# Optimization experiments

Measured on AMD Instinct MI355X. Metric: run time of the kernel, lower is better.

The kernel has to match this reference:

```python
import jax, jax.numpy as jnp
import numpy as np

N, T, DM = 8192, 32, 128   # nodes, patches, d_model (d_in = T*DM = 4096)
M, NNZ = 1024, 131072      # hyperedges, incidences
EPS = 1e-5
SLOPE = 0.2


def _bn(x, g, b, axes):
    # BatchNorm with batch statistics (training-mode math, eval dropout)
    m = jnp.mean(x, axis=axes, keepdims=True)
    v = jnp.var(x, axis=axes, keepdims=True)
    return (x - m) / jnp.sqrt(v + EPS) * g + b


def _hconv(x, he_attr, he_n, he_e, W, att, bias, heads):
    # PyG HypergraphConv, use_attention=True, attention_mode='node', concat=False
    out = W.shape[1] // heads
    xt = (x @ W).reshape(N, heads, out)          # [N, H, F]
    et = (he_attr @ W).reshape(M, heads, out)    # [M, H, F]
    xi = xt[he_n]                                # [nnz, H, F] gather node feats
    ej = et[he_e]                                # [nnz, H, F] gather edge feats
    alpha = jnp.sum(jnp.concatenate([xi, ej], axis=-1) * att, axis=-1)  # [nnz, H]
    alpha = jax.nn.leaky_relu(alpha, SLOPE)
    # segment softmax grouped by hyperedge (attention_mode='node')
    amax = jax.ops.segment_max(alpha, he_e, num_segments=M)
    ex = jnp.exp(alpha - amax[he_e])
    alpha = ex / jax.ops.segment_sum(ex, he_e, num_segments=M)[he_e]
    # degree normalizers (hyperedge_weight == 1)
    ones = jnp.ones((NNZ,), x.dtype)
    Dn = jax.ops.segment_sum(ones, he_n, num_segments=N)
    Dinv = jnp.where(Dn > 0, 1.0 / Dn, 0.0)
    Bm = jax.ops.segment_sum(ones, he_e, num_segments=M)
    Binv = jnp.where(Bm > 0, 1.0 / Bm, 0.0)
    # node -> edge, then edge -> node message passing
    eo = jax.ops.segment_sum(alpha[:, :, None] * Binv[he_e][:, None, None] * xi,
                             he_e, num_segments=M)                     # [M, H, F]
    no = jax.ops.segment_sum(alpha[:, :, None] * Dinv[he_n][:, None, None] * eo[he_e],
                             he_n, num_segments=N)                     # [N, H, F]
    return no.mean(axis=1) + bias  # concat=False -> mean over heads


def setup_inputs() -> dict:
    key = jax.random.key(0)
    ks = jax.random.split(key, 16)
    d_in = T * DM
    s = 0.02
    inp = {
        "x": jax.random.normal(ks[0], (N, T, DM), jnp.float32),
        "he_nodes": jax.random.randint(ks[1], (NNZ,), 0, N),
        "he_edges": jax.random.randint(ks[2], (NNZ,), 0, M),
        "W1": jax.random.normal(ks[3], (d_in, DM), jnp.float32) * s,
        "b1": jnp.zeros((DM,), jnp.float32),
        "g1": jnp.ones((DM,), jnp.float32), "be1": jnp.zeros((DM,), jnp.float32),
        "Wh1": jax.random.normal(ks[4], (DM, 4 * DM), jnp.float32) * s,
        "att1": jax.random.normal(ks[5], (1, 4, 2 * DM), jnp.float32) * s,
        "bh1": jnp.zeros((DM,), jnp.float32),
        "g2": jnp.ones((DM,), jnp.float32), "be2": jnp.zeros((DM,), jnp.float32),
        "Wh2": jax.random.normal(ks[6], (DM, DM), jnp.float32) * s,
        "att2": jax.random.normal(ks[7], (1, 1, 2 * DM), jnp.float32) * s,
        "bh2": jnp.zeros((DM,), jnp.float32),
        "g3": jnp.ones((DM,), jnp.float32), "be3": jnp.zeros((DM,), jnp.float32),
        "W3": jax.random.normal(ks[8], (DM, d_in), jnp.float32) * s,
        "b3": jnp.zeros((d_in,), jnp.float32),
        "g4": jnp.ones((DM,), jnp.float32), "be4": jnp.zeros((DM,), jnp.float32),
    }
    return inp


def reference(x, he_nodes, he_edges, W1, b1, g1, be1, Wh1, att1, bh1,
              g2, be2, Wh2, att2, bh2, g3, be3, W3, b3, g4, be4):
    src = x
    h = x.reshape(N, T * DM)
    h = jax.nn.leaky_relu(h @ W1 + b1, SLOPE)
    h = _bn(h, g1, be1, 0)
    # hyperedge_attr = incidence^T @ h  (== to_dense_adj(...).T @ h)
    he_attr = jax.ops.segment_sum(h[he_nodes], he_edges, num_segments=M)
    h = h + _hconv(h, he_attr, he_nodes, he_edges, Wh1, att1, bh1, 4)
    h = _bn(h, g2, be2, 0)
    he_attr = jax.ops.segment_sum(h[he_nodes], he_edges, num_segments=M)
    h = h + _hconv(h, he_attr, he_nodes, he_edges, Wh2, att2, bh2, 1)
    h = _bn(h, g3, be3, 0)
    h = jax.nn.leaky_relu(h @ W3 + b3, SLOPE)
    h = src + h.reshape(N, T, DM)
    h = _bn(h, g4, be4, (0, 1))  # BN over channel DM, stats over (N, T)
    return h
```

## Files before the change

kernel.cpp:

```cpp
#include <hip/hip_runtime.h>
#include <hip/hip_bf16.h>
#include <math.h>

#define NN   8192
#define TT   32
#define DIN  4096
#define MME  1024
#define NNZK 131072
#define EPSV 1e-5f
#define MALL (NN + MME)

typedef __attribute__((ext_vector_type(8))) short bf16x8;
typedef __attribute__((ext_vector_type(4))) float f32x4;

__device__ __forceinline__ float lrelu(float v){ return v > 0.f ? v : 0.2f*v; }
__device__ __forceinline__ short f2b(float f){
    union { __hip_bfloat16 h; short s; } u; u.h = __float2bfloat16(f); return u.s;
}

__global__ void zero_i(int* p, int n){ int i = blockIdx.x*256 + threadIdx.x; if (i < n) p[i] = 0; }
__global__ void zero_f(float* p, int n){ int i = blockIdx.x*256 + threadIdx.x; if (i < n) p[i] = 0.f; }
__global__ void copy_i(const int* a, int* b, int n){ int i = blockIdx.x*256 + threadIdx.x; if (i < n) b[i] = a[i]; }

__global__ void count_seg(const int* __restrict__ he_n, const int* __restrict__ he_e,
                          int* __restrict__ ncnt, int* __restrict__ ecnt){
    int k = blockIdx.x*256 + threadIdx.x;
    if (k < NNZK){ atomicAdd(&ecnt[he_e[k]], 1); atomicAdd(&ncnt[he_n[k]], 1); }
}

__global__ void scan_excl(const int* __restrict__ cnt, int* __restrict__ off, int n){
    __shared__ int buf[1024];
    __shared__ int carry;
    int t = threadIdx.x;
    if (t == 0) carry = 0;
    __syncthreads();
    for (int base = 0; base < n; base += 1024){
        int i = base + t;
        int v = (i < n) ? cnt[i] : 0;
        buf[t] = v; __syncthreads();
        for (int s = 1; s < 1024; s <<= 1){
            int tmp = (t >= s) ? buf[t - s] : 0;
            __syncthreads();
            buf[t] += tmp;
            __syncthreads();
        }
        if (i < n) off[i] = carry + buf[t] - v;
        __syncthreads();
        if (t == 1023) carry += buf[1023];
        __syncthreads();
    }
    if (t == 0) off[n] = carry;
}

__global__ void fill_perm(const int* __restrict__ seg, int* __restrict__ cur, int* __restrict__ perm){
    int k = blockIdx.x*256 + threadIdx.x;
    if (k < NNZK){ int p = atomicAdd(&cur[seg[k]], 1); perm[p] = k; }
}

__global__ void wconv_t(const float* __restrict__ W, __hip_bfloat16* __restrict__ BT, int K, int N){
    __shared__ float tile[32][33];
    int k0 = blockIdx.y*32, n0 = blockIdx.x*32;
    int tx = threadIdx.x & 31, ty = threadIdx.x >> 5;
    for (int i = ty; i < 32; i += 8) tile[i][tx] = W[(size_t)(k0+i)*N + n0+tx];
    __syncthreads();
    for (int i = ty; i < 32; i += 8)
        BT[(size_t)(n0+i)*K + k0 + tx] = __float2bfloat16(tile[tx][i]);
}

#define SWZ(b) ((b) ^ ((((b) >> 6) & 7) << 4))

template<int MODE>
__global__ __launch_bounds__(256) void gemm_nt(
    const float* __restrict__ Aact, const __hip_bfloat16* __restrict__ Bwt,
    float* __restrict__ C, const float* __restrict__ bias, const float* __restrict__ add,
    const float* __restrict__ coef, int M, int N, int K, int kchunk)
{
    __shared__ f32x4 WsRaw[512];
    __shared__ f32x4 XsRaw[512];
    char* Ws = (char*)WsRaw;
    char* Xs = (char*)XsRaw;
    const int tid = threadIdx.x;
    const int lane = tid & 63;
    const int w = tid >> 6;
    const int m0 = blockIdx.y << 7, n0 = blockIdx.x << 7;
    const int kz = blockIdx.z * kchunk;
    const int wN = (w >> 1) << 6, wM = (w & 1) << 6;

    const int s0 = tid, s1 = tid + 256;
    const int r0 = s0 >> 2, k0b = (s0 & 3) << 3;
    const int r1 = s1 >> 2, k1b = (s1 & 3) << 3;
    const float* pX0 = Aact + (size_t)(m0 + r0)*K + kz + k0b;
    const float* pX1 = Aact + (size_t)(m0 + r1)*K + kz + k1b;
    const __hip_bfloat16* pW0 = Bwt + (size_t)(n0 + r0)*K + kz + k0b;
    const __hip_bfloat16* pW1 = Bwt + (size_t)(n0 + r1)*K + kz + k1b;
    const int wo0 = SWZ(s0 << 4), wo1 = SWZ(s1 << 4);

    int rwOff[4], rxOff[4];
#pragma unroll
    for (int f = 0; f < 4; f++){
        rwOff[f] = SWZ((wN + f*16 + (lane & 15))*64 + ((lane >> 4) << 4));
        rxOff[f] = SWZ((wM + f*16 + (lane & 15))*64 + ((lane >> 4) << 4));
    }

    f32x4 acc[4][4] = {};

    float4 x0l = *(const float4*)pX0, x0h = *(const float4*)(pX0+4);
    float4 x1l = *(const float4*)pX1, x1h = *(const float4*)(pX1+4);
    bf16x8 w0 = *(const bf16x8*)pW0, w1 = *(const bf16x8*)pW1;

    const int nsteps = kchunk >> 5;
    for (int ks = 0; ks < nsteps; ks++){
        bf16x8 vx0, vx1;
        vx0[0]=f2b(x0l.x); vx0[1]=f2b(x0l.y); vx0[2]=f2b(x0l.z); vx0[3]=f2b(x0l.w);
        vx0[4]=f2b(x0h.x); vx0[5]=f2b(x0h.y); vx0[6]=f2b(x0h.z); vx0[7]=f2b(x0h.w);
        vx1[0]=f2b(x1l.x); vx1[1]=f2b(x1l.y); vx1[2]=f2b(x1l.z); vx1[3]=f2b(x1l.w);
        vx1[4]=f2b(x1h.x); vx1[5]=f2b(x1h.y); vx1[6]=f2b(x1h.z); vx1[7]=f2b(x1h.w);
        __syncthreads();
        *(bf16x8*)(Xs + wo0) = vx0;
        *(bf16x8*)(Xs + wo1) = vx1;
        *(bf16x8*)(Ws + wo0) = w0;
        *(bf16x8*)(Ws + wo1) = w1;
        __syncthreads();
        if (ks + 1 < nsteps){
            pX0 += 32; pX1 += 32; pW0 += 32; pW1 += 32;
            x0l = *(const float4*)pX0; x0h = *(const float4*)(pX0+4);
            x1l = *(const float4*)pX1; x1h = *(const float4*)(pX1+4);
            w0 = *(const bf16x8*)pW0;  w1 = *(const bf16x8*)pW1;
        }
        bf16x8 wf[4], xf[4];
#pragma unroll
        for (int f = 0; f < 4; f++){
            wf[f] = *(const bf16x8*)(Ws + rwOff[f]);
            xf[f] = *(const bf16x8*)(Xs + rxOff[f]);
        }
#pragma unroll
        for (int i = 0; i < 4; i++)
#pragma unroll
            for (int j = 0; j < 4; j++)
                acc[i][j] = __builtin_amdgcn_mfma_f32_16x16x32_bf16(wf[i], xf[j], acc[i][j], 0, 0, 0);
    }

    const int mc = wM + (lane & 15);
    const int ncb = wN + ((lane >> 4) << 2);
    float* Cz = (MODE == 0) ? C + (size_t)blockIdx.z * ((size_t)M * (size_t)N) : C;
#pragma unroll
    for (int j = 0; j < 4; j++){
        int row = m0 + mc + j*16;
#pragma unroll
        for (int i = 0; i < 4; i++){
            int col = n0 + ncb + i*16;
            f32x4 v = acc[i][j];
            if (MODE == 1){
                float4 b4 = *(const float4*)&bias[col];
                v[0] = lrelu(v[0] + b4.x);
                v[1] = lrelu(v[1] + b4.y);
                v[2] = lrelu(v[2] + b4.z);
                v[3] = lrelu(v[3] + b4.w);
                float4 a4 = *(const float4*)&add[(size_t)row*N + col];
                int ch = (ncb + i*16) & 127;
                float4 sc = *(const float4*)&coef[ch];
                float4 sh = *(const float4*)&coef[128 + ch];
                v[0] = (v[0] + a4.x)*sc.x + sh.x;
                v[1] = (v[1] + a4.y)*sc.y + sh.y;
                v[2] = (v[2] + a4.z)*sc.z + sh.z;
                v[3] = (v[3] + a4.w)*sc.w + sh.w;
            }
            *(float4*)&Cz[(size_t)row*N + col] = *(float4*)&v;
        }
    }
}

__global__ __launch_bounds__(256) void gemm_stats(
    const float* __restrict__ A, const __hip_bfloat16* __restrict__ BT,
    const float* __restrict__ bias, const float* __restrict__ add,
    float* __restrict__ slots, int M, int N, int K, int kchunk)
{
    __shared__ f32x4 AsRaw[512];
    __shared__ f32x4 BsRaw[512];
    char* As = (char*)AsRaw;
    char* Bs = (char*)BsRaw;
    const int tid = threadIdx.x;
    const int lane = tid & 63;
    const int w = tid >> 6;
    const int m0 = blockIdx.y << 7, n0 = blockIdx.x << 7;
    const int wr = (w >> 1) << 6, wc = (w & 1) << 6;

    const int s0 = tid, s1 = tid + 256;
    const int r0 = s0 >> 2, k0b = (s0 & 3) << 3;
    const int r1 = s1 >> 2, k1b = (s1 & 3) << 3;
    const float* pA0 = A + (size_t)(m0 + r0)*K + k0b;
    const float* pA1 = A + (size_t)(m0 + r1)*K + k1b;
    const __hip_bfloat16* pB0 = BT + (size_t)(n0 + r0)*K + k0b;
    const __hip_bfloat16* pB1 = BT + (size_t)(n0 + r1)*K + k1b;
    const int wo0 = SWZ(s0 << 4), wo1 = SWZ(s1 << 4);

    int raOff[4], rbOff[4];
#pragma unroll
    for (int f = 0; f < 4; f++){
        raOff[f] = SWZ((wr + f*16 + (lane & 15))*64 + ((lane >> 4) << 4));
        rbOff[f] = SWZ((wc + f*16 + (lane & 15))*64 + ((lane >> 4) << 4));
    }

    f32x4 acc[4][4] = {};

    float4 a0l = *(const float4*)pA0, a0h = *(const float4*)(pA0+4);
    float4 a1l = *(const float4*)pA1, a1h = *(const float4*)(pA1+4);
    bf16x8 b0 = *(const bf16x8*)pB0, b1 = *(const bf16x8*)pB1;

    const int nsteps = kchunk >> 5;
    for (int ks = 0; ks < nsteps; ks++){
        bf16x8 va0, va1;
        va0[0]=f2b(a0l.x); va0[1]=f2b(a0l.y); va0[2]=f2b(a0l.z); va0[3]=f2b(a0l.w);
        va0[4]=f2b(a0h.x); va0[5]=f2b(a0h.y); va0[6]=f2b(a0h.z); va0[7]=f2b(a0h.w);
        va1[0]=f2b(a1l.x); va1[1]=f2b(a1l.y); va1[2]=f2b(a1l.z); va1[3]=f2b(a1l.w);
        va1[4]=f2b(a1h.x); va1[5]=f2b(a1h.y); va1[6]=f2b(a1h.z); va1[7]=f2b(a1h.w);
        __syncthreads();
        *(bf16x8*)(As + wo0) = va0;
        *(bf16x8*)(As + wo1) = va1;
        *(bf16x8*)(Bs + wo0) = b0;
        *(bf16x8*)(Bs + wo1) = b1;
        __syncthreads();
        if (ks + 1 < nsteps){
            pA0 += 32; pA1 += 32; pB0 += 32; pB1 += 32;
            a0l = *(const float4*)pA0; a0h = *(const float4*)(pA0+4);
            a1l = *(const float4*)pA1; a1h = *(const float4*)(pA1+4);
            b0 = *(const bf16x8*)pB0;  b1 = *(const bf16x8*)pB1;
        }
        bf16x8 af[4], bfr[4];
#pragma unroll
        for (int f = 0; f < 4; f++){
            af[f]  = *(const bf16x8*)(As + raOff[f]);
            bfr[f] = *(const bf16x8*)(Bs + rbOff[f]);
        }
#pragma unroll
        for (int mf = 0; mf < 4; mf++)
#pragma unroll
            for (int nf = 0; nf < 4; nf++)
                acc[mf][nf] = __builtin_amdgcn_mfma_f32_16x16x32_bf16(af[mf], bfr[nf], acc[mf][nf], 0, 0, 0);
    }

    __shared__ float sS[128], sQ[128];
    if (tid < 128){ sS[tid] = 0.f; sQ[tid] = 0.f; }
    __syncthreads();
#pragma unroll
    for (int nf = 0; nf < 4; nf++){
        int lc = wc + nf*16 + (lane & 15);
        int col = n0 + lc;
        float bv = bias[col];
        float s = 0.f, q = 0.f;
#pragma unroll
        for (int mf = 0; mf < 4; mf++){
#pragma unroll
            for (int r = 0; r < 4; r++){
                int row = m0 + wr + mf*16 + ((lane >> 4) << 2) + r;
                float v = lrelu(acc[mf][nf][r] + bv) + add[(size_t)row*N + col];
                s += v; q += v*v;
            }
        }
        atomicAdd(&sS[lc & 127], s);
        atomicAdd(&sQ[lc & 127], q);
    }
    __syncthreads();
    if (tid < 128){
        atomicAdd(&slots[(blockIdx.x & 31)*256 + tid], sS[tid]);
        atomicAdd(&slots[(blockIdx.x & 31)*256 + 128 + tid], sQ[tid]);
    }
}

__global__ void reduce8s(const float* __restrict__ part, const float* __restrict__ bias,
                         float* __restrict__ out, int nf4, int parts, float* __restrict__ slots){
    int tid = threadIdx.x;
    int i = blockIdx.x*256 + tid;
    float4 s = ((const float4*)part)[i];
    for (int z = 1; z < parts; z++){
        float4 p = ((const float4*)part)[(size_t)z*nf4 + i];
        s.x += p.x; s.y += p.y; s.z += p.z; s.w += p.w;
    }
    int c0 = (i & 31) << 2;
    s.x = lrelu(s.x + bias[c0+0]); s.y = lrelu(s.y + bias[c0+1]);
    s.z = lrelu(s.z + bias[c0+2]); s.w = lrelu(s.w + bias[c0+3]);
    ((float4*)out)[i] = s;
    __shared__ float S[128], Q[128];
    if (tid < 128){ S[tid] = 0.f; Q[tid] = 0.f; }
    __syncthreads();
    atomicAdd(&S[c0+0], s.x); atomicAdd(&Q[c0+0], s.x*s.x);
    atomicAdd(&S[c0+1], s.y); atomicAdd(&Q[c0+1], s.y*s.y);
    atomicAdd(&S[c0+2], s.z); atomicAdd(&Q[c0+2], s.z*s.z);
    atomicAdd(&S[c0+3], s.w); atomicAdd(&Q[c0+3], s.w*s.w);
    __syncthreads();
    if (tid < 128){
        int slot = blockIdx.x & 31;
        atomicAdd(&slots[slot*256 + tid], S[tid]);
        atomicAdd(&slots[slot*256 + 128 + tid], Q[tid]);
    }
}

__global__ void bn_stats_v2(const float* __restrict__ x, float* __restrict__ slots, int rows){
    int cg = threadIdx.x & 31, rg = threadIdx.x >> 5;
    float4 s = {0,0,0,0}, q = {0,0,0,0};
    for (int r = blockIdx.x*8 + rg; r < rows; r += gridDim.x*8){
        float4 v = ((const float4*)x)[(size_t)r*32 + cg];
        s.x += v.x; q.x += v.x*v.x;
        s.y += v.y; q.y += v.y*v.y;
        s.z += v.z; q.z += v.z*v.z;
        s.w += v.w; q.w += v.w*v.w;
    }
    __shared__ float S[128], Q[128];
    if (threadIdx.x < 128){ S[threadIdx.x] = 0.f; Q[threadIdx.x] = 0.f; }
    __syncthreads();
    int c0 = cg << 2;
    atomicAdd(&S[c0+0], s.x); atomicAdd(&Q[c0+0], q.x);
    atomicAdd(&S[c0+1], s.y); atomicAdd(&Q[c0+1], q.y);
    atomicAdd(&S[c0+2], s.z); atomicAdd(&Q[c0+2], q.z);
    atomicAdd(&S[c0+3], s.w); atomicAdd(&Q[c0+3], q.w);
    __syncthreads();
    if (threadIdx.x < 128){
        int slot = blockIdx.x & 31;
        atomicAdd(&slots[slot*256 + threadIdx.x], S[threadIdx.x]);
        atomicAdd(&slots[slot*256 + 128 + threadIdx.x], Q[threadIdx.x]);
    }
}

__global__ void bn_finalize2(const float* __restrict__ slots, int nslots,
                             const float* __restrict__ g, const float* __restrict__ b,
                             float invR, float* __restrict__ coef){
    int c = threadIdx.x;
    float s = 0.f, q = 0.f;
    for (int k = 0; k < nslots; k++){ s += slots[k*256 + c]; q += slots[k*256 + 128 + c]; }
    float m = s*invR;
    float v = q*invR - m*m;
    float sc = g[c]*rsqrtf(v + EPSV);
    coef[c] = sc;
    coef[128 + c] = b[c] - m*sc;
}

__global__ void bn_apply4(float4* __restrict__ x, const float* __restrict__ coef, size_t n4){
    size_t i = (size_t)blockIdx.x*blockDim.x + threadIdx.x;
    size_t stride = (size_t)gridDim.x*blockDim.x;
    for (; i < n4; i += stride){
        int c0 = (int)(i & 31) * 4;
        float4 v = x[i];
        v.x = v.x*coef[c0+0] + coef[128+c0+0];
        v.y = v.y*coef[c0+1] + coef[128+c0+1];
        v.z = v.z*coef[c0+2] + coef[128+c0+2];
        v.w = v.w*coef[c0+3] + coef[128+c0+3];
        x[i] = v;
    }
}

__global__ void seg_sum_edge(const int* __restrict__ eoff, const int* __restrict__ eperm,
                             const int* __restrict__ he_n, const float* __restrict__ h,
                             float* __restrict__ out){
    int m = blockIdx.x, c = threadIdx.x;
    int s0 = eoff[m], cnt = eoff[m+1] - s0;
    __shared__ int sn[128];
    float acc = 0.f;
    for (int base = 0; base < cnt; base += 128){
        int i = base + c;
        if (i < cnt) sn[c] = he_n[eperm[s0+i]];
        __syncthreads();
        int lim = min(128, cnt - base);
        for (int j = 0; j < lim; j++) acc += h[(size_t)sn[j]*128 + c];
        __syncthreads();
    }
    out[(size_t)m*128 + c] = acc;
}

template<int H>
__global__ void row_att(const float* __restrict__ xt, const float* __restrict__ att,
                        int aoff, float* __restrict__ out){
    int n = blockIdx.x, lane = threadIdx.x;
#pragma unroll
    for (int h = 0; h < H; h++){
        const float* xr = xt + (size_t)n*(H*128) + h*128;
        const float* ar = att + h*256 + aoff;
        float s = xr[lane]*ar[lane] + xr[lane+64]*ar[lane+64];
        for (int d = 32; d > 0; d >>= 1) s += __shfl_down(s, d);
        if (lane == 0) out[n*H + h] = s;
    }
}

template<int H>
__global__ void seg_softmax(const int* __restrict__ eoff, const int* __restrict__ eperm,
                            const int* __restrict__ he_n,
                            const float* __restrict__ ax, const float* __restrict__ ae,
                            float* __restrict__ alpha){
    int m = blockIdx.x, t = threadIdx.x;
    int s0 = eoff[m], cnt = eoff[m+1] - s0;
    if (cnt == 0) return;
    __shared__ float red[128];
    float aeh[H];
#pragma unroll
    for (int h = 0; h < H; h++) aeh[h] = ae[m*H + h];
    float lmax[H];
#pragma unroll
    for (int h = 0; h < H; h++) lmax[h] = -1e30f;
    for (int i = t; i < cnt; i += 128){
        int k = eperm[s0+i]; int n = he_n[k];
#pragma unroll
        for (int h = 0; h < H; h++){
            float v = lrelu(ax[n*H + h] + aeh[h]);
            alpha[(size_t)k*H + h] = v;
            lmax[h] = fmaxf(lmax[h], v);
        }
    }
    float gmax[H];
#pragma unroll
    for (int h = 0; h < H; h++){
        red[t] = lmax[h]; __syncthreads();
        for (int s = 64; s > 0; s >>= 1){ if (t < s) red[t] = fmaxf(red[t], red[t+s]); __syncthreads(); }
        gmax[h] = red[0]; __syncthreads();
    }
    float lsum[H];
#pragma unroll
    for (int h = 0; h < H; h++) lsum[h] = 0.f;
    for (int i = t; i < cnt; i += 128){
        int k = eperm[s0+i];
#pragma unroll
        for (int h = 0; h < H; h++){
            float ex = __expf(alpha[(size_t)k*H + h] - gmax[h]);
            alpha[(size_t)k*H + h] = ex;
            lsum[h] += ex;
        }
    }
    float ginv[H];
#pragma unroll
    for (int h = 0; h < H; h++){
        red[t] = lsum[h]; __syncthreads();
        for (int s = 64; s > 0; s >>= 1){ if (t < s) red[t] += red[t+s]; __syncthreads(); }
        ginv[h] = 1.f/red[0]; __syncthreads();
    }
    for (int i = t; i < cnt; i += 128){
        int k = eperm[s0+i];
#pragma unroll
        for (int h = 0; h < H; h++) alpha[(size_t)k*H + h] *= ginv[h];
    }
}

__global__ void seg_eo4(const int* __restrict__ eoff, const int* __restrict__ eperm,
                        const int* __restrict__ he_n,
                        const float* __restrict__ alpha, const float* __restrict__ xt,
                        float* __restrict__ eo){
    int m = blockIdx.x;
    int c = threadIdx.x & 127, hb = threadIdx.x >> 7;
    int s0 = eoff[m], cnt = eoff[m+1] - s0;
    __shared__ int sn[128];
    __shared__ float sa[128][4];
    float acc0 = 0.f, acc1 = 0.f;
    for (int base = 0; base < cnt; base += 128){
        int i = base + threadIdx.x;
        if (threadIdx.x < 128 && i < cnt){
            int k = eperm[s0+i];
            sn[threadIdx.x] = he_n[k];
#pragma unroll
            for (int h = 0; h < 4; h++) sa[threadIdx.x][h] = alpha[(size_t)k*4 + h];
        }
        __syncthreads();
        int lim = min(128, cnt - base);
        for (int j = 0; j < lim; j++){
            const float* xr = xt + (size_t)sn[j]*512;
            acc0 += sa[j][hb]   * xr[hb*128 + c];
            acc1 += sa[j][hb+2] * xr[(hb+2)*128 + c];
        }
        __syncthreads();
    }
    float binv = cnt > 0 ? 1.f/(float)cnt : 0.f;
    eo[(size_t)m*512 + hb*128 + c]     = acc0*binv;
    eo[(size_t)m*512 + (hb+2)*128 + c] = acc1*binv;
}

__global__ void seg_eo1(const int* __restrict__ eoff, const int* __restrict__ eperm,
                        const int* __restrict__ he_n,
                        const float* __restrict__ alpha, const float* __restrict__ xt,
                        float* __restrict__ eo){
    int m = blockIdx.x, c = threadIdx.x;
    int s0 = eoff[m], cnt = eoff[m+1] - s0;
    __shared__ int sn[128];
    __shared__ float sa[128];
    float acc = 0.f;
    for (int base = 0; base < cnt; base += 128){
        int i = base + c;
        if (i < cnt){
            int k = eperm[s0+i];
            sn[c] = he_n[k];
            sa[c] = alpha[k];
        }
        __syncthreads();
        int lim = min(128, cnt - base);
        for (int j = 0; j < lim; j++) acc += sa[j]*xt[(size_t)sn[j]*128 + c];
        __syncthreads();
    }
    float binv = cnt > 0 ? 1.f/(float)cnt : 0.f;
    eo[(size_t)m*128 + c] = acc*binv;
}

template<int H>
__global__ void seg_node_out(const int* __restrict__ noff, const int* __restrict__ nperm,
                             const int* __restrict__ he_e,
                             const float* __restrict__ alpha, const float* __restrict__ eo,
                             const float* __restrict__ hin, const float* __restrict__ bias,
                             float* __restrict__ hout){
    int n = blockIdx.x, c = threadIdx.x;
    int s0 = noff[n], cnt = noff[n+1] - s0;
    float acc = 0.f;
    for (int i = 0; i < cnt; i++){
        int k = nperm[s0+i]; int e = he_e[k];
        const float* er = eo + (size_t)e*(128*H);
#pragma unroll
        for (int h = 0; h < H; h++) acc += alpha[(size_t)k*H + h]*er[h*128 + c];
    }
    float dinv = cnt > 0 ? 1.f/((float)cnt*(float)H) : 0.f;
    hout[(size_t)n*128 + c] = hin[(size_t)n*128 + c] + bias[c] + acc*dinv;
}

extern "C" void kernel_launch(void* const* d_in, const int* in_sizes, int n_in,
                              void* d_out, int out_size, void* d_ws, size_t ws_size,
                              hipStream_t stream){
    const float* x    = (const float*)d_in[0];
    const int*   he_n = (const int*)  d_in[1];
    const int*   he_e = (const int*)  d_in[2];
    const float* W1   = (const float*)d_in[3];
    const float* b1   = (const float*)d_in[4];
    const float* g1   = (const float*)d_in[5];
    const float* be1  = (const float*)d_in[6];
    const float* Wh1  = (const float*)d_in[7];
    const float* att1 = (const float*)d_in[8];
    const float* bh1  = (const float*)d_in[9];
    const float* g2   = (const float*)d_in[10];
    const float* be2  = (const float*)d_in[11];
    const float* Wh2  = (const float*)d_in[12];
    const float* att2 = (const float*)d_in[13];
    const float* bh2  = (const float*)d_in[14];
    const float* g3   = (const float*)d_in[15];
    const float* be3  = (const float*)d_in[16];
    const float* W3   = (const float*)d_in[17];
    const float* b3   = (const float*)d_in[18];
    const float* g4   = (const float*)d_in[19];
    const float* be4  = (const float*)d_in[20];
    float* out = (float*)d_out;

    char* ws = (char*)d_ws;
    size_t off = 0;
    auto alloc = [&](size_t bytes)->char*{ char* p = ws + off; off += (bytes + 255) & ~(size_t)255; return p; };

    float* hall1  = (float*)alloc((size_t)MALL*128*4);
    float* hall2  = (float*)alloc((size_t)MALL*128*4);
    float* h3     = (float*)alloc((size_t)NN*128*4);
    float* xt1    = (float*)alloc((size_t)MALL*512*4);
    float* xt2    = (float*)alloc((size_t)MALL*128*4);
    float* eo     = (float*)alloc((size_t)MME*512*4);
    float* alpha  = (float*)alloc((size_t)NNZK*4*4);
    float* ax     = (float*)alloc((size_t)NN*4*4);
    float* ae     = (float*)alloc((size_t)MME*4*4);
    float* slots  = (float*)alloc((size_t)32*256*4);
    float* coef   = (float*)alloc(256*4);
    float* part   = (float*)alloc((size_t)8*NN*128*4);
    __hip_bfloat16* W1T  = (__hip_bfloat16*)alloc((size_t)128*DIN*2);
    __hip_bfloat16* Wh1T = (__hip_bfloat16*)alloc((size_t)512*128*2);
    __hip_bfloat16* Wh2T = (__hip_bfloat16*)alloc((size_t)128*128*2);
    __hip_bfloat16* W3T  = (__hip_bfloat16*)alloc((size_t)DIN*128*2);
    int* ecnt  = (int*)alloc(MME*4);
    int* ncnt  = (int*)alloc(NN*4);
    int* eoffb = (int*)alloc((MME+1)*4);
    int* ecur  = (int*)alloc(MME*4);
    int* noffb = (int*)alloc((NN+1)*4);
    int* ncur  = (int*)alloc(NN*4);
    int* eperm = (int*)alloc((size_t)NNZK*4);
    int* nperm = (int*)alloc((size_t)NNZK*4);

    zero_i<<<(MME+NN+255)/256, 256, 0, stream>>>(ecnt, MME+NN);
    count_seg<<<NNZK/256, 256, 0, stream>>>(he_n, he_e, ncnt, ecnt);
    scan_excl<<<1, 1024, 0, stream>>>(ecnt, eoffb, MME);
    scan_excl<<<1, 1024, 0, stream>>>(ncnt, noffb, NN);
    copy_i<<<(MME+255)/256, 256, 0, stream>>>(eoffb, ecur, MME);
    copy_i<<<(NN+255)/256, 256, 0, stream>>>(noffb, ncur, NN);
    fill_perm<<<NNZK/256, 256, 0, stream>>>(he_e, ecur, eperm);
    fill_perm<<<NNZK/256, 256, 0, stream>>>(he_n, ncur, nperm);

    wconv_t<<<dim3(128/32, DIN/32), 256, 0, stream>>>(W1,  W1T,  DIN, 128);
    wconv_t<<<dim3(512/32, 128/32), 256, 0, stream>>>(Wh1, Wh1T, 128, 512);
    wconv_t<<<dim3(128/32, 128/32), 256, 0, stream>>>(Wh2, Wh2T, 128, 128);
    wconv_t<<<dim3(DIN/32, 128/32), 256, 0, stream>>>(W3,  W3T,  128, DIN);

    gemm_nt<0><<<dim3(1, NN/128, 8), 256, 0, stream>>>(x, W1T, part, nullptr, nullptr, nullptr, NN, 128, DIN, DIN/8);
    zero_f<<<32, 256, 0, stream>>>(slots, 32*256);
    reduce8s<<<NN*128/4/256, 256, 0, stream>>>(part, b1, hall1, NN*128/4, 8, slots);
    bn_finalize2<<<1, 128, 0, stream>>>(slots, 32, g1, be1, 1.f/NN, coef);
    bn_apply4<<<1024, 256, 0, stream>>>((float4*)hall1, coef, (size_t)NN*32);

    seg_sum_edge<<<MME, 128, 0, stream>>>(eoffb, eperm, he_n, hall1, hall1 + (size_t)NN*128);
    gemm_nt<0><<<dim3(512/128, MALL/128, 1), 256, 0, stream>>>(hall1, Wh1T, xt1, nullptr, nullptr, nullptr, MALL, 512, 128, 128);
    row_att<4><<<NN, 64, 0, stream>>>(xt1, att1, 0, ax);
    row_att<4><<<MME, 64, 0, stream>>>(xt1 + (size_t)NN*512, att1, 128, ae);
    seg_softmax<4><<<MME, 128, 0, stream>>>(eoffb, eperm, he_n, ax, ae, alpha);
    seg_eo4<<<MME, 256, 0, stream>>>(eoffb, eperm, he_n, alpha, xt1, eo);
    seg_node_out<4><<<NN, 128, 0, stream>>>(noffb, nperm, he_e, alpha, eo, hall1, bh1, hall2);
    zero_f<<<32, 256, 0, stream>>>(slots, 32*256);
    bn_stats_v2<<<256, 256, 0, stream>>>(hall2, slots, NN);
    bn_finalize2<<<1, 128, 0, stream>>>(slots, 32, g2, be2, 1.f/NN, coef);
    bn_apply4<<<1024, 256, 0, stream>>>((float4*)hall2, coef, (size_t)NN*32);

    seg_sum_edge<<<MME, 128, 0, stream>>>(eoffb, eperm, he_n, hall2, hall2 + (size_t)NN*128);
    gemm_nt<0><<<dim3(1, MALL/128, 1), 256, 0, stream>>>(hall2, Wh2T, xt2, nullptr, nullptr, nullptr, MALL, 128, 128, 128);
    row_att<1><<<NN, 64, 0, stream>>>(xt2, att2, 0, ax);
    row_att<1><<<MME, 64, 0, stream>>>(xt2 + (size_t)NN*128, att2, 128, ae);
    seg_softmax<1><<<MME, 128, 0, stream>>>(eoffb, eperm, he_n, ax, ae, alpha);
    seg_eo1<<<MME, 128, 0, stream>>>(eoffb, eperm, he_n, alpha, xt2, eo);
    seg_node_out<1><<<NN, 128, 0, stream>>>(noffb, nperm, he_e, alpha, eo, hall2, bh2, h3);
    zero_f<<<32, 256, 0, stream>>>(slots, 32*256);
    bn_stats_v2<<<256, 256, 0, stream>>>(h3, slots, NN);
    bn_finalize2<<<1, 128, 0, stream>>>(slots, 32, g3, be3, 1.f/NN, coef);
    bn_apply4<<<1024, 256, 0, stream>>>((float4*)h3, coef, (size_t)NN*32);

    zero_f<<<32, 256, 0, stream>>>(slots, 32*256);
    gemm_stats<<<dim3(DIN/128, NN/128), 256, 0, stream>>>(h3, W3T, b3, x, slots, NN, DIN, 128, 128);
    bn_finalize2<<<1, 128, 0, stream>>>(slots, 32, g4, be4, 1.f/((float)NN*TT), coef);
    gemm_nt<1><<<dim3(DIN/128, NN/128, 1), 256, 0, stream>>>(h3, W3T, out, b3, x, coef, NN, DIN, 128, 128);
}
```

Baseline: 526.7 us.

## Compute W3 GEMM once into bf16 buffer, split final BN into stats/apply passes

Previously the final W3 GEMM ran twice: once to collect BatchNorm statistics and once to apply them. Now it runs once and stores leaky-relu output as bf16, and two streaming kernels compute the statistics and apply the normalization with the residual. The first GEMM's split-K partials are also stored as bf16 with 16 splits instead of 8 fp32 splits, sharing one workspace with xt1. This trades redundant MFMA work for an extra bf16 round trip through memory and adds bf16 rounding of intermediates.

```diff
diff --git a/kernel.cpp b/kernel.cpp
--- a/kernel.cpp
+++ b/kernel.cpp
@@ -16,6 +16,9 @@
 __device__ __forceinline__ float lrelu(float v){ return v > 0.f ? v : 0.2f*v; }
 __device__ __forceinline__ short f2b(float f){
     union { __hip_bfloat16 h; short s; } u; u.h = __float2bfloat16(f); return u.s;
+}
+__device__ __forceinline__ float b2f(short s){
+    union { float f; unsigned u; } u; u.u = ((unsigned)(unsigned short)s) << 16; return u.f;
 }
 
 __global__ void zero_i(int* p, int n){ int i = blockIdx.x*256 + threadIdx.x; if (i < n) p[i] = 0; }
@@ -72,8 +75,8 @@
 template<int MODE>
 __global__ __launch_bounds__(256) void gemm_nt(
     const float* __restrict__ Aact, const __hip_bfloat16* __restrict__ Bwt,
-    float* __restrict__ C, const float* __restrict__ bias, const float* __restrict__ add,
-    const float* __restrict__ coef, int M, int N, int K, int kchunk)
+    float* __restrict__ C, __hip_bfloat16* __restrict__ Cb, const float* __restrict__ bias,
+    int M, int N, int K, int kchunk)
 {
     __shared__ f32x4 WsRaw[512];
     __shared__ f32x4 XsRaw[512];
@@ -142,7 +145,6 @@
 
     const int mc = wM + (lane & 15);
     const int ncb = wN + ((lane >> 4) << 2);
-    float* Cz = (MODE == 0) ? C + (size_t)blockIdx.z * ((size_t)M * (size_t)N) : C;
 #pragma unroll
     for (int j = 0; j < 4; j++){
         int row = m0 + mc + j*16;
@@ -150,131 +152,32 @@
         for (int i = 0; i < 4; i++){
             int col = n0 + ncb + i*16;
             f32x4 v = acc[i][j];
-            if (MODE == 1){
+            if (MODE == 0){
+                *(float4*)&C[(size_t)row*N + col] = *(float4*)&v;
+            } else if (MODE == 2){
+                __hip_bfloat16* Cz = Cb + (size_t)blockIdx.z * ((size_t)M * (size_t)N);
+                short4 sv = { f2b(v[0]), f2b(v[1]), f2b(v[2]), f2b(v[3]) };
+                *(short4*)&Cz[(size_t)row*N + col] = sv;
+            } else {
                 float4 b4 = *(const float4*)&bias[col];
-                v[0] = lrelu(v[0] + b4.x);
-                v[1] = lrelu(v[1] + b4.y);
-                v[2] = lrelu(v[2] + b4.z);
-                v[3] = lrelu(v[3] + b4.w);
-                float4 a4 = *(const float4*)&add[(size_t)row*N + col];
-                int ch = (ncb + i*16) & 127;
-                float4 sc = *(const float4*)&coef[ch];
-                float4 sh = *(const float4*)&coef[128 + ch];
-                v[0] = (v[0] + a4.x)*sc.x + sh.x;
-                v[1] = (v[1] + a4.y)*sc.y + sh.y;
-                v[2] = (v[2] + a4.z)*sc.z + sh.z;
-                v[3] = (v[3] + a4.w)*sc.w + sh.w;
+                short4 sv = { f2b(lrelu(v[0] + b4.x)), f2b(lrelu(v[1] + b4.y)),
+                              f2b(lrelu(v[2] + b4.z)), f2b(lrelu(v[3] + b4.w)) };
+                *(short4*)&Cb[(size_t)row*N + col] = sv;
             }
-            *(float4*)&Cz[(size_t)row*N + col] = *(float4*)&v;
-        }
-    }
-}
-
-__global__ __launch_bounds__(256) void gemm_stats(
-    const float* __restrict__ A, const __hip_bfloat16* __restrict__ BT,
-    const float* __restrict__ bias, const float* __restrict__ add,
-    float* __restrict__ slots, int M, int N, int K, int kchunk)
-{
-    __shared__ f32x4 AsRaw[512];
-    __shared__ f32x4 BsRaw[512];
-    char* As = (char*)AsRaw;
-    char* Bs = (char*)BsRaw;
-    const int tid = threadIdx.x;
-    const int lane = tid & 63;
-    const int w = tid >> 6;
-    const int m0 = blockIdx.y << 7, n0 = blockIdx.x << 7;
-    const int wr = (w >> 1) << 6, wc = (w & 1) << 6;
-
-    const int s0 = tid, s1 = tid + 256;
-    const int r0 = s0 >> 2, k0b = (s0 & 3) << 3;
-    const int r1 = s1 >> 2, k1b = (s1 & 3) << 3;
-    const float* pA0 = A + (size_t)(m0 + r0)*K + k0b;
-    const float* pA1 = A + (size_t)(m0 + r1)*K + k1b;
-    const __hip_bfloat16* pB0 = BT + (size_t)(n0 + r0)*K + k0b;
-    const __hip_bfloat16* pB1 = BT + (size_t)(n0 + r1)*K + k1b;
-    const int wo0 = SWZ(s0 << 4), wo1 = SWZ(s1 << 4);
-
-    int raOff[4], rbOff[4];
-#pragma unroll
-    for (int f = 0; f < 4; f++){
-        raOff[f] = SWZ((wr + f*16 + (lane & 15))*64 + ((lane >> 4) << 4));
-        rbOff[f] = SWZ((wc + f*16 + (lane & 15))*64 + ((lane >> 4) << 4));
-    }
-
-    f32x4 acc[4][4] = {};
-
-    float4 a0l = *(const float4*)pA0, a0h = *(const float4*)(pA0+4);
-    float4 a1l = *(const float4*)pA1, a1h = *(const float4*)(pA1+4);
-    bf16x8 b0 = *(const bf16x8*)pB0, b1 = *(const bf16x8*)pB1;
-
-    const int nsteps = kchunk >> 5;
-    for (int ks = 0; ks < nsteps; ks++){
-        bf16x8 va0, va1;
-        va0[0]=f2b(a0l.x); va0[1]=f2b(a0l.y); va0[2]=f2b(a0l.z); va0[3]=f2b(a0l.w);
-        va0[4]=f2b(a0h.x); va0[5]=f2b(a0h.y); va0[6]=f2b(a0h.z); va0[7]=f2b(a0h.w);
-        va1[0]=f2b(a1l.x); va1[1]=f2b(a1l.y); va1[2]=f2b(a1l.z); va1[3]=f2b(a1l.w);
-        va1[4]=f2b(a1h.x); va1[5]=f2b(a1h.y); va1[6]=f2b(a1h.z); va1[7]=f2b(a1h.w);
-        __syncthreads();
-        *(bf16x8*)(As + wo0) = va0;
-        *(bf16x8*)(As + wo1) = va1;
-        *(bf16x8*)(Bs + wo0) = b0;
-        *(bf16x8*)(Bs + wo1) = b1;
-        __syncthreads();
-        if (ks + 1 < nsteps){
-            pA0 += 32; pA1 += 32; pB0 += 32; pB1 += 32;
-            a0l = *(const float4*)pA0; a0h = *(const float4*)(pA0+4);
-            a1l = *(const float4*)pA1; a1h = *(const float4*)(pA1+4);
-            b0 = *(const bf16x8*)pB0;  b1 = *(const bf16x8*)pB1;
-        }
-        bf16x8 af[4], bfr[4];
-#pragma unroll
-        for (int f = 0; f < 4; f++){
-            af[f]  = *(const bf16x8*)(As + raOff[f]);
-            bfr[f] = *(const bf16x8*)(Bs + rbOff[f]);
-        }
-#pragma unroll
-        for (int mf = 0; mf < 4; mf++)
-#pragma unroll
-            for (int nf = 0; nf < 4; nf++)
-                acc[mf][nf] = __builtin_amdgcn_mfma_f32_16x16x32_bf16(af[mf], bfr[nf], acc[mf][nf], 0, 0, 0);
-    }
-
-    __shared__ float sS[128], sQ[128];
-    if (tid < 128){ sS[tid] = 0.f; sQ[tid] = 0.f; }
-    __syncthreads();
-#pragma unroll
-    for (int nf = 0; nf < 4; nf++){
-        int lc = wc + nf*16 + (lane & 15);
-        int col = n0 + lc;
-        float bv = bias[col];
-        float s = 0.f, q = 0.f;
-#pragma unroll
-        for (int mf = 0; mf < 4; mf++){
-#pragma unroll
-            for (int r = 0; r < 4; r++){
-                int row = m0 + wr + mf*16 + ((lane >> 4) << 2) + r;
-                float v = lrelu(acc[mf][nf][r] + bv) + add[(size_t)row*N + col];
-                s += v; q += v*v;
-            }
-        }
-        atomicAdd(&sS[lc & 127], s);
-        atomicAdd(&sQ[lc & 127], q);
-    }
-    __syncthreads();
-    if (tid < 128){
-        atomicAdd(&slots[(blockIdx.x & 31)*256 + tid], sS[tid]);
-        atomicAdd(&slots[(blockIdx.x & 31)*256 + 128 + tid], sQ[tid]);
-    }
-}
-
-__global__ void reduce8s(const float* __restrict__ part, const float* __restrict__ bias,
+        }
+    }
+}
+
+__global__ void reduce8s(const __hip_bfloat16* __restrict__ part, const float* __restrict__ bias,
                          float* __restrict__ out, int nf4, int parts, float* __restrict__ slots){
     int tid = threadIdx.x;
     int i = blockIdx.x*256 + tid;
-    float4 s = ((const float4*)part)[i];
+    const short4* p4 = (const short4*)part;
+    short4 v0 = p4[i];
+    float4 s = { b2f(v0.x), b2f(v0.y), b2f(v0.z), b2f(v0.w) };
     for (int z = 1; z < parts; z++){
-        float4 p = ((const float4*)part)[(size_t)z*nf4 + i];
-        s.x += p.x; s.y += p.y; s.z += p.z; s.w += p.w;
+        short4 p = p4[(size_t)z*nf4 + i];
+        s.x += b2f(p.x); s.y += b2f(p.y); s.z += b2f(p.z); s.w += b2f(p.w);
     }
     int c0 = (i & 31) << 2;
     s.x = lrelu(s.x + bias[c0+0]); s.y = lrelu(s.y + bias[c0+1]);
@@ -292,6 +195,58 @@
         int slot = blockIdx.x & 31;
         atomicAdd(&slots[slot*256 + tid], S[tid]);
         atomicAdd(&slots[slot*256 + 128 + tid], Q[tid]);
+    }
+}
+
+__global__ __launch_bounds__(256) void final_stats(
+    const float4* __restrict__ x, const short4* __restrict__ f,
+    float* __restrict__ slots, int n4)
+{
+    int tid = threadIdx.x;
+    float4 s = {0,0,0,0}, q = {0,0,0,0};
+    int stride = gridDim.x*256;
+    for (int i = blockIdx.x*256 + tid; i < n4; i += stride){
+        float4 xv = x[i]; short4 fv = f[i];
+        float y0 = xv.x + b2f(fv.x), y1 = xv.y + b2f(fv.y);
+        float y2 = xv.z + b2f(fv.z), y3 = xv.w + b2f(fv.w);
+        s.x += y0; q.x += y0*y0;
+        s.y += y1; q.y += y1*y1;
+        s.z += y2; q.z += y2*y2;
+        s.w += y3; q.w += y3*y3;
+    }
+    __shared__ float S[128], Q[128];
+    if (tid < 128){ S[tid] = 0.f; Q[tid] = 0.f; }
+    __syncthreads();
+    int c0 = (tid & 31) << 2;
+    atomicAdd(&S[c0+0], s.x); atomicAdd(&Q[c0+0], q.x);
+    atomicAdd(&S[c0+1], s.y); atomicAdd(&Q[c0+1], q.y);
+    atomicAdd(&S[c0+2], s.z); atomicAdd(&Q[c0+2], q.z);
+    atomicAdd(&S[c0+3], s.w); atomicAdd(&Q[c0+3], q.w);
+    __syncthreads();
+    if (tid < 128){
+        int slot = blockIdx.x & 31;
+        atomicAdd(&slots[slot*256 + tid], S[tid]);
+        atomicAdd(&slots[slot*256 + 128 + tid], Q[tid]);
+    }
+}
+
+__global__ __launch_bounds__(256) void final_apply(
+    const float4* __restrict__ x, const short4* __restrict__ f,
+    const float* __restrict__ coef, float4* __restrict__ out, int n4)
+{
+    int tid = threadIdx.x;
+    int c0 = (tid & 31) << 2;
+    float4 sc = *(const float4*)&coef[c0];
+    float4 sh = *(const float4*)&coef[128 + c0];
+    int stride = gridDim.x*256;
+    for (int i = blockIdx.x*256 + tid; i < n4; i += stride){
+        float4 xv = x[i]; short4 fv = f[i];
+        float4 v;
+        v.x = (xv.x + b2f(fv.x))*sc.x + sh.x;
+        v.y = (xv.y + b2f(fv.y))*sc.y + sh.y;
+        v.z = (xv.z + b2f(fv.z))*sc.z + sh.z;
+        v.w = (xv.w + b2f(fv.w))*sc.w + sh.w;
+        out[i] = v;
     }
 }
 
@@ -543,10 +498,14 @@
     size_t off = 0;
     auto alloc = [&](size_t bytes)->char*{ char* p = ws + off; off += (bytes + 255) & ~(size_t)255; return p; };
 
+    char* big = alloc((size_t)NN*DIN*2);
+    __hip_bfloat16* fbuf = (__hip_bfloat16*)big;
+    __hip_bfloat16* part = (__hip_bfloat16*)big;
+    float*          xt1  = (float*)(big + (size_t)16*NN*128*2);
+
     float* hall1  = (float*)alloc((size_t)MALL*128*4);
     float* hall2  = (float*)alloc((size_t)MALL*128*4);
     float* h3     = (float*)alloc((size_t)NN*128*4);
-    float* xt1    = (float*)alloc((size_t)MALL*512*4);
     float* xt2    = (float*)alloc((size_t)MALL*128*4);
     float* eo     = (float*)alloc((size_t)MME*512*4);
     float* alpha  = (float*)alloc((size_t)NNZK*4*4);
@@ -554,7 +513,6 @@
     float* ae     = (float*)alloc((size_t)MME*4*4);
     float* slots  = (float*)alloc((size_t)32*256*4);
     float* coef   = (float*)alloc(256*4);
-    float* part   = (float*)alloc((size_t)8*NN*128*4);
     __hip_bfloat16* W1T  = (__hip_bfloat16*)alloc((size_t)128*DIN*2);
     __hip_bfloat16* Wh1T = (__hip_bfloat16*)alloc((size_t)512*128*2);
     __hip_bfloat16* Wh2T = (__hip_bfloat16*)alloc((size_t)128*128*2);
@@ -582,14 +540,14 @@
     wconv_t<<<dim3(128/32, 128/32), 256, 0, stream>>>(Wh2, Wh2T, 128, 128);
     wconv_t<<<dim3(DIN/32, 128/32), 256, 0, stream>>>(W3,  W3T,  128, DIN);
 
-    gemm_nt<0><<<dim3(1, NN/128, 8), 256, 0, stream>>>(x, W1T, part, nullptr, nullptr, nullptr, NN, 128, DIN, DIN/8);
+    gemm_nt<2><<<dim3(1, NN/128, 16), 256, 0, stream>>>(x, W1T, nullptr, part, nullptr, NN, 128, DIN, DIN/16);
     zero_f<<<32, 256, 0, stream>>>(slots, 32*256);
-    reduce8s<<<NN*128/4/256, 256, 0, stream>>>(part, b1, hall1, NN*128/4, 8, slots);
+    reduce8s<<<NN*128/4/256, 256, 0, stream>>>(part, b1, hall1, NN*128/4, 16, slots);
     bn_finalize2<<<1, 128, 0, stream>>>(slots, 32, g1, be1, 1.f/NN, coef);
     bn_apply4<<<1024, 256, 0, stream>>>((float4*)hall1, coef, (size_t)NN*32);
 
     seg_sum_edge<<<MME, 128, 0, stream>>>(eoffb, eperm, he_n, hall1, hall1 + (size_t)NN*128);
-    gemm_nt<0><<<dim3(512/128, MALL/128, 1), 256, 0, stream>>>(hall1, Wh1T, xt1, nullptr, nullptr, nullptr, MALL, 512, 128, 128);
+    gemm_nt<0><<<dim3(512/128, MALL/128, 1), 256, 0, stream>>>(hall1, Wh1T, xt1, nullptr, nullptr, MALL, 512, 128, 128);
     row_att<4><<<NN, 64, 0, stream>>>(xt1, att1, 0, ax);
     row_att<4><<<MME, 64, 0, stream>>>(xt1 + (size_t)NN*512, att1, 128, ae);
     seg_softmax<4><<<MME, 128, 0, stream>>>(eoffb, eperm, he_n, ax, ae, alpha);
@@ -601,7 +559,7 @@
     bn_apply4<<<1024, 256, 0, stream>>>((float4*)hall2, coef, (size_t)NN*32);
 
     seg_sum_edge<<<MME, 128, 0, stream>>>(eoffb, eperm, he_n, hall2, hall2 + (size_t)NN*128);
-    gemm_nt<0><<<dim3(1, MALL/128, 1), 256, 0, stream>>>(hall2, Wh2T, xt2, nullptr, nullptr, nullptr, MALL, 128, 128, 128);
+    gemm_nt<0><<<dim3(1, MALL/128, 1), 256, 0, stream>>>(hall2, Wh2T, xt2, nullptr, nullptr, MALL, 128, 128, 128);
     row_att<1><<<NN, 64, 0, stream>>>(xt2, att2, 0, ax);
     row_att<1><<<MME, 64, 0, stream>>>(xt2 + (size_t)NN*128, att2, 128, ae);
     seg_softmax<1><<<MME, 128, 0, stream>>>(eoffb, eperm, he_n, ax, ae, alpha);
@@ -612,8 +570,9 @@
     bn_finalize2<<<1, 128, 0, stream>>>(slots, 32, g3, be3, 1.f/NN, coef);
     bn_apply4<<<1024, 256, 0, stream>>>((float4*)h3, coef, (size_t)NN*32);
 
+    gemm_nt<3><<<dim3(DIN/128, NN/128, 1), 256, 0, stream>>>(h3, W3T, nullptr, fbuf, b3, NN, DIN, 128, 128);
     zero_f<<<32, 256, 0, stream>>>(slots, 32*256);
-    gemm_stats<<<dim3(DIN/128, NN/128), 256, 0, stream>>>(h3, W3T, b3, x, slots, NN, DIN, 128, 128);
+    final_stats<<<2048, 256, 0, stream>>>((const float4*)x, (const short4*)fbuf, slots, NN*TT*32);
     bn_finalize2<<<1, 128, 0, stream>>>(slots, 32, g4, be4, 1.f/((float)NN*TT), coef);
-    gemm_nt<1><<<dim3(DIN/128, NN/128, 1), 256, 0, stream>>>(h3, W3T, out, b3, x, coef, NN, DIN, 128, 128);
-}
+    final_apply<<<2048, 256, 0, stream>>>((const float4*)x, (const short4*)fbuf, coef, (float4*)out, NN*TT*32);
+}
```

Result: slower. 562.8 us (+6.8%).
